# Optimization experiments

Hardware: AMD Instinct MI355X
Metric: run time of the kernel (lower is better)

The kernel has to match this reference:

```python
import jax, jax.numpy as jnp
import numpy as np

VOL_DIM = 256  # stored volume is [256,256,256,1]


def _deform(c, W1, b1, W2, b2, W3, b3, Wf, bf):
    # chain of 1x1x1 convs (== per-voxel matmuls) with cos activations, residual *5
    h = jnp.cos(jnp.einsum('...c,cd->...d', c, W1) + b1)
    h = jnp.cos(jnp.einsum('...c,cd->...d', h, W2) + b2)
    h = jnp.cos(jnp.einsum('...c,cd->...d', h, W3) + b3)
    return c + 5.0 * (jnp.einsum('...c,cd->...d', h, Wf) + bf)


def _trilinear_sample(vol, coords):
    # vol: [X,Y,Z,C]; coords: [...,3] in voxel units (identity nifti edges)
    X, Y, Z, _ = vol.shape
    hi = jnp.array([X - 1, Y - 1, Z - 1], dtype=coords.dtype)
    c = jnp.clip(coords, 0.0, hi)
    c0 = jnp.floor(c)
    f = c - c0
    i0 = c0.astype(jnp.int32)
    i1 = jnp.minimum(i0 + 1, jnp.array([X - 1, Y - 1, Z - 1], jnp.int32))
    x0, y0, z0 = i0[..., 0], i0[..., 1], i0[..., 2]
    x1, y1, z1 = i1[..., 0], i1[..., 1], i1[..., 2]
    fx, fy, fz = f[..., 0:1], f[..., 1:2], f[..., 2:3]
    gx, gy, gz = 1.0 - fx, 1.0 - fy, 1.0 - fz
    out = (vol[x0, y0, z0] * (gx * gy * gz) + vol[x1, y0, z0] * (fx * gy * gz)
         + vol[x0, y1, z0] * (gx * fy * gz) + vol[x0, y0, z1] * (gx * gy * fz)
         + vol[x1, y1, z0] * (fx * fy * gz) + vol[x1, y0, z1] * (fx * gy * fz)
         + vol[x0, y1, z1] * (gx * fy * fz) + vol[x1, y1, z1] * (fx * fy * fz))
    return out  # [...,C]


def setup_inputs() -> dict:
    key = jax.random.key(0)
    ks = jax.random.split(key, 12)
    B, P = 64, 32
    # coords in [0, 255] world==voxel units; extra intensity channel (unused by call)
    coords = jax.random.uniform(ks[0], (B, P, P, P, 3), jnp.float32) * (VOL_DIM - 1.0)
    inten = jax.random.normal(ks[1], (B, P, P, P, 1), jnp.float32)
    x = jnp.concatenate([coords, inten], axis=-1)
    s = 0.1
    return {
        'x': x,
        'W1': jax.random.normal(ks[2], (3, 32), jnp.float32) * s,
        'b1': jax.random.normal(ks[3], (32,), jnp.float32) * s,
        'W2': jax.random.normal(ks[4], (32, 32), jnp.float32) * s,
        'b2': jax.random.normal(ks[5], (32,), jnp.float32) * s,
        'W3': jax.random.normal(ks[6], (32, 32), jnp.float32) * s,
        'b3': jax.random.normal(ks[7], (32,), jnp.float32) * s,
        'Wf': jax.random.normal(ks[8], (32, 3), jnp.float32) * s,
        'bf': jax.random.normal(ks[9], (3,), jnp.float32) * s,
        'vol': jax.random.normal(ks[10], (VOL_DIM, VOL_DIM, VOL_DIM, 1), jnp.float32),
    }


def reference(x, W1, b1, W2, b2, W3, b3, Wf, bf, vol):
    c = x[..., 0:3]                                   # world coords
    c = _deform(c, W1, b1, W2, b2, W3, b3, Wf, bf)    # deformed coords
    return _trilinear_sample(vol, c)                  # [B,32,32,32,1]
```

## Files before the change

### kernel.cpp

```cpp
#include <hip/hip_runtime.h>


#define NPTS (64 * 32 * 32 * 32)
#define NBLK (NPTS / 256)
#define SSTR 40

typedef __attribute__((ext_vector_type(8))) short bf16x8;
typedef __attribute__((ext_vector_type(4))) short s16x4;
typedef __attribute__((ext_vector_type(4))) float f32x4;
typedef unsigned long long u64;
typedef unsigned short u16;

__device__ __forceinline__ short bf16rne(float f) {
    unsigned u = __builtin_bit_cast(unsigned, f);
    return (short)((u + 0x7fffu + ((u >> 16) & 1u)) >> 16);
}
__device__ __forceinline__ float bf16tof(short s) {
    return __builtin_bit_cast(float, ((unsigned)(unsigned short)s) << 16);
}
__device__ __forceinline__ float h2f(u16 h) {
    return (float)__builtin_bit_cast(_Float16, h);
}
__device__ __forceinline__ u16 f2h(float f) {
    return __builtin_bit_cast(u16, (_Float16)f);
}

__global__ __launch_bounds__(256)
void retile_k(const float4* __restrict__ vol, u64* __restrict__ dst) {
    int t   = blockIdx.x * 256 + threadIdx.x;
    int q   = t & 7;
    int gz  = (t >> 3) & 63;
    int gyx = t >> 9;
    int x = ((gyx >> 7) << 2) + (q >> 1);
    int y = ((gyx & 127) << 1) + (q & 1);
    float4 v = vol[(((x << 8) + y) << 6) + gz];
    u64 r =  (u64)f2h(v.x)
          | ((u64)f2h(v.y) << 16)
          | ((u64)f2h(v.z) << 32)
          | ((u64)f2h(v.w) << 48);
    dst[t] = r;
}

template <int BRICK>
__global__ __launch_bounds__(256, 8)
void deform_sample_k(const float4* __restrict__ x,
                     const float4* __restrict__ W1,
                     const float4* __restrict__ b1,
                     const float*  __restrict__ W2,
                     const float*  __restrict__ b2,
                     const float*  __restrict__ W3,
                     const float*  __restrict__ b3,
                     const float*  __restrict__ Wf,
                     const float*  __restrict__ bf_,
                     const float*  __restrict__ volf,
                     const u64*    __restrict__ volh,
                     float* __restrict__ out)
{
    __shared__ short lds[4 * 64 * SSTR];
    const int tid  = threadIdx.x;
    const int lane = tid & 63;
    const int wv   = tid >> 6;
    const int m16  = lane & 15;
    const int q    = lane >> 4;
    short* __restrict__ L = &lds[wv * 64 * SSTR];

    const int p = blockIdx.x * 256 + tid;

    const float4 xv = x[p];
    const float c0 = xv.x, c1 = xv.y, c2 = xv.z;

    {
        bf16x8 hw;
        #pragma unroll
        for (int j4 = 0; j4 < 8; ++j4) {
            float4 wa = W1[j4], wb = W1[8 + j4], wc = W1[16 + j4], bb = b1[j4];
            float v0 = __cosf(fmaf(c0, wa.x, fmaf(c1, wb.x, fmaf(c2, wc.x, bb.x))));
            float v1 = __cosf(fmaf(c0, wa.y, fmaf(c1, wb.y, fmaf(c2, wc.y, bb.y))));
            float v2 = __cosf(fmaf(c0, wa.z, fmaf(c1, wb.z, fmaf(c2, wc.z, bb.z))));
            float v3 = __cosf(fmaf(c0, wa.w, fmaf(c1, wb.w, fmaf(c2, wc.w, bb.w))));
            int o = (j4 & 1) * 4;
            hw[o+0] = bf16rne(v0); hw[o+1] = bf16rne(v1);
            hw[o+2] = bf16rne(v2); hw[o+3] = bf16rne(v3);
            if (j4 & 1)
                *(bf16x8*)&L[lane * SSTR + (j4 - 1) * 4] = hw;
        }
    }
    __syncthreads();

    const float* const Wly[2] = { W2, W3 };
    const float* const bly[2] = { b2, b3 };
    #pragma unroll
    for (int ly = 0; ly < 2; ++ly) {
        const float* __restrict__ W  = Wly[ly];
        const float* __restrict__ bb = bly[ly];
        bf16x8 A0, A1;
        #pragma unroll
        for (int j = 0; j < 8; ++j) {
            A0[j] = bf16rne(W[(q * 8 + j) * 32 + m16]);
            A1[j] = bf16rne(W[(q * 8 + j) * 32 + 16 + m16]);
        }
        const float4 blo = *(const float4*)&bb[q * 4];
        const float4 bhi = *(const float4*)&bb[16 + q * 4];

        #pragma unroll
        for (int t = 0; t < 4; ++t) {
            bf16x8 bfrag = *(const bf16x8*)&L[(t * 16 + m16) * SSTR + q * 8];
            f32x4 z = { 0.f, 0.f, 0.f, 0.f };
            f32x4 d0 = __builtin_amdgcn_mfma_f32_16x16x32_bf16(A0, bfrag, z, 0, 0, 0);
            f32x4 d1 = __builtin_amdgcn_mfma_f32_16x16x32_bf16(A1, bfrag, z, 0, 0, 0);

            s16x4 w0, w1;
            w0[0] = bf16rne(__cosf(d0[0] + blo.x));
            w0[1] = bf16rne(__cosf(d0[1] + blo.y));
            w0[2] = bf16rne(__cosf(d0[2] + blo.z));
            w0[3] = bf16rne(__cosf(d0[3] + blo.w));
            w1[0] = bf16rne(__cosf(d1[0] + bhi.x));
            w1[1] = bf16rne(__cosf(d1[1] + bhi.y));
            w1[2] = bf16rne(__cosf(d1[2] + bhi.z));
            w1[3] = bf16rne(__cosf(d1[3] + bhi.w));
            *(s16x4*)&L[(t * 16 + m16) * SSTR + q * 4]      = w0;
            *(s16x4*)&L[(t * 16 + m16) * SSTR + 16 + q * 4] = w1;
        }
        __syncthreads();
    }

    float d0 = bf_[0], d1 = bf_[1], d2 = bf_[2];
    #pragma unroll
    for (int j4 = 0; j4 < 8; ++j4) {
        s16x4 v = *(const s16x4*)&L[lane * SSTR + j4 * 4];
        #pragma unroll
        for (int r = 0; r < 4; ++r) {
            float hv = bf16tof(v[r]);
            int ii = j4 * 4 + r;
            d0 = fmaf(hv, Wf[3*ii+0], d0);
            d1 = fmaf(hv, Wf[3*ii+1], d1);
            d2 = fmaf(hv, Wf[3*ii+2], d2);
        }
    }
    float e0 = fmaf(5.f, d0, c0);
    float e1 = fmaf(5.f, d1, c1);
    float e2 = fmaf(5.f, d2, c2);

    e0 = fminf(fmaxf(e0, 0.f), 255.f);
    e1 = fminf(fmaxf(e1, 0.f), 255.f);
    e2 = fminf(fmaxf(e2, 0.f), 255.f);
    float fl0 = floorf(e0), fl1 = floorf(e1), fl2 = floorf(e2);
    float fx = e0 - fl0, fy = e1 - fl1, fz = e2 - fl2;
    float gx = 1.f - fx, gy = 1.f - fy, gz = 1.f - fz;
    int x0 = (int)fl0, y0 = (int)fl1, z0 = (int)fl2;
    int x1 = min(x0 + 1, 255), y1 = min(y0 + 1, 255), z1 = min(z0 + 1, 255);

    float v000, v001, v010, v011, v100, v101, v110, v111;

    if constexpr (BRICK) {
        const int lz  = z0 & 3;
        const int zp  = (z0 >> 2) << 6;
        const int xp0 = ((x0 >> 2) << 19) | ((x0 & 3) << 4);
        const int xp1 = ((x1 >> 2) << 19) | ((x1 & 3) << 4);
        const int yp0 = ((y0 >> 1) << 12) | ((y0 & 1) << 3);
        const int yp1 = ((y1 >> 1) << 12) | ((y1 & 1) << 3);
        const char* vb = (const char*)volh;
        const int a00 = xp0 | yp0 | zp, a10 = xp1 | yp0 | zp;
        const int a01 = xp0 | yp1 | zp, a11 = xp1 | yp1 | zp;
        u64 L00 = *(const u64*)(vb + a00);
        u64 L10 = *(const u64*)(vb + a10);
        u64 L01 = *(const u64*)(vb + a01);
        u64 L11 = *(const u64*)(vb + a11);
        u64 H00 = 0, H10 = 0, H01 = 0, H11 = 0;
        const bool crossz = (lz == 3) && (z0 < 255);
        if (crossz) {
            H00 = *(const u64*)(vb + a00 + 64);
            H10 = *(const u64*)(vb + a10 + 64);
            H01 = *(const u64*)(vb + a01 + 64);
            H11 = *(const u64*)(vb + a11 + 64);
        }
        const int sh = lz * 16;
        const bool in_line = (lz < 3);
        auto ext = [&](u64 lo, u64 hi, float& a, float& b) {
            u64 s = lo >> sh;
            a = h2f((u16)s);
            float b_in = h2f((u16)(s >> 16));
            float b_nx = h2f((u16)hi);
            b = in_line ? b_in : (crossz ? b_nx : a);
        };
        ext(L00, H00, v000, v001);
        ext(L10, H10, v100, v101);
        ext(L01, H01, v010, v011);
        ext(L11, H11, v110, v111);
    } else {
        int b00 = (x0 << 16) | (y0 << 8);
        int b01 = (x0 << 16) | (y1 << 8);
        int b10 = (x1 << 16) | (y0 << 8);
        int b11 = (x1 << 16) | (y1 << 8);
        v000 = volf[b00 + z0]; v001 = volf[b00 + z1];
        v010 = volf[b01 + z0]; v011 = volf[b01 + z1];
        v100 = volf[b10 + z0]; v101 = volf[b10 + z1];
        v110 = volf[b11 + z0]; v111 = volf[b11 + z1];
    }

    float r = gz * (gy * (gx*v000 + fx*v100) + fy * (gx*v010 + fx*v110))
            + fz * (gy * (gx*v001 + fx*v101) + fy * (gx*v011 + fx*v111));

    out[p] = r;
}

extern "C" void kernel_launch(void* const* d_in, const int* in_sizes, int n_in,
                              void* d_out, int out_size, void* d_ws, size_t ws_size,
                              hipStream_t stream) {
    const float4* x   = (const float4*)d_in[0];
    const float4* W1  = (const float4*)d_in[1];
    const float4* b1  = (const float4*)d_in[2];
    const float*  W2  = (const float*)d_in[3];
    const float*  b2  = (const float*)d_in[4];
    const float*  W3  = (const float*)d_in[5];
    const float*  b3  = (const float*)d_in[6];
    const float*  Wf  = (const float*)d_in[7];
    const float*  bf_ = (const float*)d_in[8];
    const float*  vol = (const float*)d_in[9];
    float* out = (float*)d_out;

    const size_t need = (size_t)4194304 * 8;
    if (ws_size >= need) {
        u64* volh = (u64*)d_ws;
        retile_k<<<16384, 256, 0, stream>>>((const float4*)vol, volh);
        deform_sample_k<1><<<NBLK, 256, 0, stream>>>(x, W1, b1, W2, b2, W3, b3,
                                                     Wf, bf_, nullptr, volh, out);
    } else {
        deform_sample_k<0><<<NBLK, 256, 0, stream>>>(x, W1, b1, W2, b2, W3, b3,
                                                     Wf, bf_, vol, nullptr, out);
    }
}
```

Measured before the change: 213.1 us.

## Retile volume into overlapping halo bricks so each sample hits one cache line

After: 213.4 us. Within noise of the previous version (+0.1%).

```diff
diff --git a/kernel.cpp b/kernel.cpp
--- a/kernel.cpp
+++ b/kernel.cpp
@@ -4,6 +4,13 @@
 #define NPTS (64 * 32 * 32 * 32)
 #define NBLK (NPTS / 256)
 #define SSTR 40
+
+#define BXN 86
+#define BYN 128
+#define BZN 86
+#define NBRICK (BXN * BYN * BZN)
+#define RETILE_T (NBRICK * 8)
+#define RETILE_BLK (RETILE_T / 256)
 
 typedef __attribute__((ext_vector_type(8))) short bf16x8;
 typedef __attribute__((ext_vector_type(4))) short s16x4;
@@ -41,7 +48,31 @@
     dst[t] = r;
 }
 
-template <int BRICK>
+__global__ __launch_bounds__(256)
+void retile_halo_k(const float* __restrict__ vol, u64* __restrict__ dst) {
+    int t  = blockIdx.x * 256 + threadIdx.x;
+    int q  = t & 7;
+    int b  = t >> 3;
+    int bz = (int)((unsigned)b % 86u);
+    int r  = (int)((unsigned)b / 86u);
+    int by = r & 127;
+    int bx = r >> 7;
+    int x  = min(bx * 3 + (q >> 1), 255);
+    int y  = (by << 1) + (q & 1);
+    int z0 = bz * 3;
+    const float* row = vol + (((x << 8) + y) << 8);
+    float v0 = row[z0];
+    float v1 = row[min(z0 + 1, 255)];
+    float v2 = row[min(z0 + 2, 255)];
+    float v3 = row[min(z0 + 3, 255)];
+    u64 rr = (u64)f2h(v0)
+          | ((u64)f2h(v1) << 16)
+          | ((u64)f2h(v2) << 32)
+          | ((u64)f2h(v3) << 48);
+    dst[t] = rr;
+}
+
+template <int MODE>
 __global__ __launch_bounds__(256, 8)
 void deform_sample_k(const float4* __restrict__ x,
                      const float4* __restrict__ W1,
@@ -152,7 +183,29 @@
 
     float v000, v001, v010, v011, v100, v101, v110, v111;
 
-    if constexpr (BRICK) {
+    if constexpr (MODE == 2) {
+        int bx = (int)((unsigned)x0 / 3u);  int lx = x0 - bx * 3;
+        int by = y0 >> 1;                   int ly = y0 & 1;
+        int bz = (int)((unsigned)z0 / 3u);  int lz = z0 - bz * 3;
+        const char* vb = (const char*)volh;
+        const int lineA = ((((bx << 7) + by) * 86) + bz) << 6;
+        const int byB   = min(by + 1, 127);
+        const int lineB = (ly == 0) ? lineA
+                                    : (((((bx << 7) + byB) * 86) + bz) << 6);
+        const int yrowB = (ly == 0) ? 1 : ((y0 == 255) ? 1 : 0);
+        const int offA  = lx * 16 + ly * 8;
+        const int offB  = lx * 16 + yrowB * 8;
+        u64 LA0 = *(const u64*)(vb + lineA + offA);
+        u64 LA1 = *(const u64*)(vb + lineA + offA + 16);
+        u64 LB0 = *(const u64*)(vb + lineB + offB);
+        u64 LB1 = *(const u64*)(vb + lineB + offB + 16);
+        const int sh = lz * 16;
+        u64 sA0 = LA0 >> sh, sA1 = LA1 >> sh, sB0 = LB0 >> sh, sB1 = LB1 >> sh;
+        v000 = h2f((u16)sA0);  v001 = h2f((u16)(sA0 >> 16));
+        v100 = h2f((u16)sA1);  v101 = h2f((u16)(sA1 >> 16));
+        v010 = h2f((u16)sB0);  v011 = h2f((u16)(sB0 >> 16));
+        v110 = h2f((u16)sB1);  v111 = h2f((u16)(sB1 >> 16));
+    } else if constexpr (MODE == 1) {
         const int lz  = z0 & 3;
         const int zp  = (z0 >> 2) << 6;
         const int xp0 = ((x0 >> 2) << 19) | ((x0 & 3) << 4);
@@ -219,8 +272,14 @@
     const float*  vol = (const float*)d_in[9];
     float* out = (float*)d_out;
 
-    const size_t need = (size_t)4194304 * 8;
-    if (ws_size >= need) {
+    const size_t needH = (size_t)NBRICK * 64;
+    const size_t need1 = (size_t)4194304 * 8;
+    if (ws_size >= needH) {
+        u64* volh = (u64*)d_ws;
+        retile_halo_k<<<RETILE_BLK, 256, 0, stream>>>(vol, volh);
+        deform_sample_k<2><<<NBLK, 256, 0, stream>>>(x, W1, b1, W2, b2, W3, b3,
+                                                     Wf, bf_, nullptr, volh, out);
+    } else if (ws_size >= need1) {
         u64* volh = (u64*)d_ws;
         retile_k<<<16384, 256, 0, stream>>>((const float4*)vol, volh);
         deform_sample_k<1><<<NBLK, 256, 0, stream>>>(x, W1, b1, W2, b2, W3, b3,
```
